# Kernel tuning notes

Hardware: AMD Instinct MI355X
Metric: run time of the kernel (lower is better)

## Reference

```python
import jax, jax.numpy as jnp
import numpy as np
import math

B, S, D, H, HD, BS = 8, 1024, 1024, 16, 64, 8  # batch, seq, dim, heads, head_dim, blk_size
ROPE_BASE = 10000.0


def setup_inputs() -> dict:
    key = jax.random.key(0)
    ks = jax.random.split(key, 5)
    std = 1.0 / math.sqrt(D)
    x = jax.random.normal(ks[0], (B, S, D), dtype=jnp.float32)
    wq = jax.random.normal(ks[1], (D, D), dtype=jnp.float32) * std
    wk = jax.random.normal(ks[2], (D, D), dtype=jnp.float32) * std
    wv = jax.random.normal(ks[3], (D, D), dtype=jnp.float32) * std
    wo = jax.random.normal(ks[4], (D, D), dtype=jnp.float32) * std
    inv_freq = 1.0 / (ROPE_BASE ** (np.arange(0, HD, 2, dtype=np.float32) / HD))
    ang = np.outer(np.arange(S, dtype=np.float32), inv_freq)  # (S, HD/2)
    freqs_cos = jnp.asarray(np.cos(ang), dtype=jnp.float32)
    freqs_sin = jnp.asarray(np.sin(ang), dtype=jnp.float32)
    return {"x": x, "wq": wq, "wk": wk, "wv": wv, "wo": wo,
            "freqs_cos": freqs_cos, "freqs_sin": freqs_sin}


def _rope(t, cos, sin):
    # t: (B, S, H, HD); cos/sin: (S, HD/2); complex-pair rotary (interleaved)
    tr, ti = t[..., 0::2], t[..., 1::2]
    c = cos[None, :, None, :]
    s = sin[None, :, None, :]
    out_r = tr * c - ti * s
    out_i = tr * s + ti * c
    return jnp.stack([out_r, out_i], axis=-1).reshape(t.shape)


def reference(x, wq, wk, wv, wo, freqs_cos, freqs_sin):
    b, s, _ = x.shape
    q = (x @ wq).reshape(b, s, H, HD)
    k = (x @ wk).reshape(b, s, H, HD)
    v = (x @ wv).reshape(b, s, H, HD)
    q = _rope(q, freqs_cos, freqs_sin)
    k = _rope(k, freqs_cos, freqs_sin)
    # block-causal mask: query attends to any key whose block index <= its own
    pos = jnp.arange(s)
    allowed = (pos[None, :] // BS) <= (pos[:, None] // BS)  # (S, S)
    scale = 1.0 / math.sqrt(HD)
    scores = jnp.einsum("bqhd,bkhd->bhqk", q, k) * scale
    scores = jnp.where(allowed[None, None], scores, jnp.finfo(scores.dtype).min)
    probs = jax.nn.softmax(scores, axis=-1)
    out = jnp.einsum("bhqk,bkhd->bqhd", probs, v).reshape(b, s, H * HD)
    return out @ wo
```

## Files before the change

kernel.cpp:

```cpp
#include <hip/hip_runtime.h>
#include <stdint.h>

#define BATCH 8
#define SEQ 1024
#define DMODEL 1024
#define NHEAD 16
#define HDIM 64
#define MROWS (BATCH * SEQ)
#define NQKV (3 * DMODEL)
#define SCALE_LOG2E 0.18033688011112043f

typedef __bf16 bf16x8 __attribute__((ext_vector_type(8)));
typedef float f32x4 __attribute__((ext_vector_type(4)));
typedef unsigned short u16x8 __attribute__((ext_vector_type(8)));
typedef unsigned short u16x4 __attribute__((ext_vector_type(4)));

static __device__ __forceinline__ unsigned short f2bf(float f) {
  unsigned int u = __builtin_bit_cast(unsigned int, f);
  u += 0x7fffu + ((u >> 16) & 1u);
  return (unsigned short)(u >> 16);
}
static __device__ __forceinline__ float bf2f(unsigned short h) {
  unsigned int u = ((unsigned int)h) << 16;
  return __builtin_bit_cast(float, u);
}
static __device__ __forceinline__ void async_cp16(void* lds, const void* g) {
  __builtin_amdgcn_global_load_lds((const __attribute__((address_space(1))) void*)g,
                                   (__attribute__((address_space(3))) void*)lds, 16, 0, 0);
}

__global__ void k_cvt_x(const float* __restrict__ x, unsigned short* __restrict__ xb) {
  const size_t i = ((size_t)blockIdx.x * 256 + threadIdx.x) * 4;
  const float4 v = *(const float4*)(x + i);
  u16x4 o;
  o[0] = f2bf(v.x); o[1] = f2bf(v.y); o[2] = f2bf(v.z); o[3] = f2bf(v.w);
  *(u16x4*)(xb + i) = o;
}

__global__ void k_tpose_tab(const float* __restrict__ fc, const float* __restrict__ fs,
                            float* __restrict__ fcT, float* __restrict__ fsT) {
  const int i = blockIdx.x * 256 + threadIdx.x;
  const int pr = i >> 10, s = i & 1023;
  fcT[i] = fc[s * 32 + pr];
  fsT[i] = fs[s * 32 + pr];
}

__global__ void k_cvt_w(const float* __restrict__ wq, const float* __restrict__ wk,
                        const float* __restrict__ wv, const float* __restrict__ wo,
                        unsigned short* __restrict__ wqkvT, unsigned short* __restrict__ woT) {
  __shared__ float tile[64][65];
  const int z = blockIdx.z;
  const float* w = (z == 0) ? wq : (z == 1) ? wk : (z == 2) ? wv : wo;
  unsigned short* dst = (z < 3) ? (wqkvT + (size_t)z * DMODEL * DMODEL) : woT;
  const int n0 = blockIdx.x * 64, k0 = blockIdx.y * 64;
  for (int i = threadIdx.x; i < 4096; i += 256) {
    const int r = i >> 6, c = i & 63;
    tile[r][c] = w[(size_t)(k0 + r) * DMODEL + n0 + c];
  }
  __syncthreads();
  for (int i = threadIdx.x; i < 4096; i += 256) {
    const int r = i >> 6, c = i & 63;
    dst[(size_t)(n0 + r) * DMODEL + k0 + c] = f2bf(tile[c][r]);
  }
}

template <int NOUT, bool F32OUT>
__global__ __launch_bounds__(256) void k_gemm(const unsigned short* __restrict__ A,
                                              const unsigned short* __restrict__ Bt,
                                              void* __restrict__ Cout) {
  constexpr int K = DMODEL;
  constexpr int GX = NOUT / 128;
  __shared__ unsigned short Al[128 * 32];
  __shared__ unsigned short Bl[128 * 32];
  const int nwg = gridDim.x;
  const int o = blockIdx.x;
  const int t = (o & 7) * (nwg >> 3) + (o >> 3);
  const int tm = (t / GX) * 128, tn = (t % GX) * 128;
  const int tid = threadIdx.x;
  const int lane = tid & 63, wid = tid >> 6;
  const int wm = wid >> 1, wn = wid & 1;
  const int fr = lane & 15, fq = lane >> 4;

  f32x4 acc[4][4];
#pragma unroll
  for (int i = 0; i < 4; ++i)
#pragma unroll
    for (int j = 0; j < 4; ++j) acc[i][j] = (f32x4){0.f, 0.f, 0.f, 0.f};

  const int o0 = wid * 2048 + lane * 16;
  const int row0 = o0 >> 6;
  const int ce0 = (o0 & 63) >> 1;

  for (int kk = 0; kk < K; kk += 32) {
    async_cp16((char*)Al + wid * 2048,        A + (size_t)(tm + row0) * K + kk + ce0);
    async_cp16((char*)Al + wid * 2048 + 1024, A + (size_t)(tm + row0 + 16) * K + kk + ce0);
    async_cp16((char*)Bl + wid * 2048,        Bt + (size_t)(tn + row0) * K + kk + ce0);
    async_cp16((char*)Bl + wid * 2048 + 1024, Bt + (size_t)(tn + row0 + 16) * K + kk + ce0);
    __syncthreads();
    bf16x8 af[4], bf[4];
#pragma unroll
    for (int mi = 0; mi < 4; ++mi)
      af[mi] = *(const bf16x8*)(Al + (wm * 64 + mi * 16 + fr) * 32 + fq * 8);
#pragma unroll
    for (int ni = 0; ni < 4; ++ni)
      bf[ni] = *(const bf16x8*)(Bl + (wn * 64 + ni * 16 + fr) * 32 + fq * 8);
#pragma unroll
    for (int mi = 0; mi < 4; ++mi)
#pragma unroll
      for (int ni = 0; ni < 4; ++ni)
        acc[mi][ni] = __builtin_amdgcn_mfma_f32_16x16x32_bf16(af[mi], bf[ni], acc[mi][ni], 0, 0, 0);
    __syncthreads();
  }

#pragma unroll
  for (int mi = 0; mi < 4; ++mi) {
    const int row = tm + wm * 64 + mi * 16 + fq * 4;
#pragma unroll
    for (int ni = 0; ni < 4; ++ni) {
      const int col = tn + wn * 64 + ni * 16 + fr;
      if constexpr (F32OUT) {
        float* C = (float*)Cout;
#pragma unroll
        for (int r = 0; r < 4; ++r) C[(size_t)(row + r) * NOUT + col] = acc[mi][ni][r];
      } else {
        unsigned short* C = (unsigned short*)Cout;
#pragma unroll
        for (int r = 0; r < 4; ++r) C[(size_t)(row + r) * NOUT + col] = f2bf(acc[mi][ni][r]);
      }
    }
  }
}

__global__ __launch_bounds__(256, 3) void k_gemm_qkv(const unsigned short* __restrict__ A,
                                                     const unsigned short* __restrict__ Bt,
                                                     const float* __restrict__ fcT,
                                                     const float* __restrict__ fsT,
                                                     unsigned short* __restrict__ qr,
                                                     unsigned short* __restrict__ kr,
                                                     unsigned short* __restrict__ vt) {
  constexpr int K = DMODEL;
  constexpr int GX = NQKV / 128;
  __shared__ unsigned short Al[128 * 32];
  __shared__ unsigned short Bl[128 * 32];
  const int nwg = gridDim.x;
  const int o = blockIdx.x;
  const int t = (o & 7) * (nwg >> 3) + (o >> 3);
  const int tm = (t / GX) * 128, tn = (t % GX) * 128;
  const int tid = threadIdx.x;
  const int lane = tid & 63, wid = tid >> 6;
  const int wm = wid >> 1, wn = wid & 1;
  const int fr = lane & 15, fq = lane >> 4;

  f32x4 acc[4][4];
#pragma unroll
  for (int i = 0; i < 4; ++i)
#pragma unroll
    for (int j = 0; j < 4; ++j) acc[i][j] = (f32x4){0.f, 0.f, 0.f, 0.f};

  const int o0 = wid * 2048 + lane * 16;
  const int row0 = o0 >> 6;
  const int ce0 = (o0 & 63) >> 1;

  for (int kk = 0; kk < K; kk += 32) {
    async_cp16((char*)Al + wid * 2048,        A + (size_t)(tm + row0) * K + kk + ce0);
    async_cp16((char*)Al + wid * 2048 + 1024, A + (size_t)(tm + row0 + 16) * K + kk + ce0);
    async_cp16((char*)Bl + wid * 2048,        Bt + (size_t)(tn + row0) * K + kk + ce0);
    async_cp16((char*)Bl + wid * 2048 + 1024, Bt + (size_t)(tn + row0 + 16) * K + kk + ce0);
    __syncthreads();
    bf16x8 af[4], bf[4];
#pragma unroll
    for (int mi = 0; mi < 4; ++mi)
      af[mi] = *(const bf16x8*)(Al + (wm * 64 + mi * 16 + fr) * 32 + fq * 8);
#pragma unroll
    for (int ni = 0; ni < 4; ++ni)
      bf[ni] = *(const bf16x8*)(Bl + (wn * 64 + ni * 16 + fr) * 32 + fq * 8);
#pragma unroll
    for (int mi = 0; mi < 4; ++mi)
#pragma unroll
      for (int ni = 0; ni < 4; ++ni)
        acc[mi][ni] = __builtin_amdgcn_mfma_f32_16x16x32_bf16(af[mi], bf[ni], acc[mi][ni], 0, 0, 0);
    __syncthreads();
  }

  const int typ = tn >> 10;
  const int hh = ((tn & 1023) >> 6) + wn;
  if (typ == 2) {
#pragma unroll
    for (int mi = 0; mi < 4; ++mi) {
      const int rowb = tm + wm * 64 + mi * 16 + fq * 4;
      const int b = rowb >> 10, s0 = rowb & 1023;
#pragma unroll
      for (int ni = 0; ni < 4; ++ni) {
        const int hd = ni * 16 + fr;
        u16x4 ov;
#pragma unroll
        for (int r = 0; r < 4; ++r) ov[r] = f2bf(acc[mi][ni][r]);
        *(u16x4*)(vt + ((size_t)((b * 16 + hh) * 64 + hd)) * SEQ + s0) = ov;
      }
    }
  } else {
    unsigned short* dst = (typ == 0) ? qr : kr;
    const float sgn = (fr & 1) ? 1.0f : -1.0f;
#pragma unroll
    for (int mi = 0; mi < 4; ++mi) {
      const int rowb = tm + wm * 64 + mi * 16 + fq * 4;
      const int b = rowb >> 10, s0 = rowb & 1023;
#pragma unroll
      for (int ni = 0; ni < 4; ++ni) {
        const int hd = ni * 16 + fr;
        const int pr = ni * 8 + (fr >> 1);
        const f32x4 cc = *(const f32x4*)(fcT + (pr << 10) + s0);
        const f32x4 ss = *(const f32x4*)(fsT + (pr << 10) + s0);
#pragma unroll
        for (int r = 0; r < 4; ++r) {
          const float a = acc[mi][ni][r];
          const float p = __shfl_xor(a, 1);
          dst[((size_t)((b * 16 + hh) * SEQ) + s0 + r) * HDIM + hd] = f2bf(a * cc[r] + sgn * (p * ss[r]));
        }
      }
    }
  }
}

__global__ __launch_bounds__(256) void k_attn(const unsigned short* __restrict__ qr,
                                              const unsigned short* __restrict__ kr,
                                              const unsigned short* __restrict__ vt,
                                              unsigned short* __restrict__ ao) {
  const int o = blockIdx.x, nwg = gridDim.x;
  const int t = (o & 7) * (nwg >> 3) + (o >> 3);
  const int qt = 15 - (t & 15);
  const int bh = t >> 4;
  const int tid = threadIdx.x, lane = tid & 63, w = tid >> 6;
  const int fr = lane & 15, fq = lane >> 4;
  __shared__ unsigned short Ks[2][4096];
  __shared__ unsigned short Vs[2][4096];
  __shared__ unsigned short Ps[4][1024];
  const size_t base = (size_t)bh * SEQ * HDIM;
  const char* kgb = (const char*)(kr + base);
  const char* vgb = (const char*)(vt + base);

  const int qrow = qt * 64 + w * 16 + fr;
  const bf16x8 qf0 = *(const bf16x8*)(qr + base + (size_t)qrow * HDIM + fq * 8);
  const bf16x8 qf1 = *(const bf16x8*)(qr + base + (size_t)qrow * HDIM + 32 + fq * 8);
  const int qblk = (w * 16 + fr) >> 3;
  const int swz = (fr & 7) << 4;

  f32x4 oacc[4];
#pragma unroll
  for (int i = 0; i < 4; ++i) oacc[i] = (f32x4){0.f, 0.f, 0.f, 0.f};
  float m = -3.0e38f, l = 0.f;

  auto stage = [&](int kt, int bb) {
#pragma unroll
    for (int c = 0; c < 2; ++c) {
      const int dstb = c * 4096 + tid * 16;
      const int row = dstb >> 7;
      const int col = (dstb & 127) ^ ((row & 7) << 4);
      char* kl = (char*)Ks[bb] + c * 4096 + (tid >> 6) * 1024;
      char* vl = (char*)Vs[bb] + c * 4096 + (tid >> 6) * 1024;
      async_cp16(kl, kgb + (size_t)kt * 8192 + row * 128 + col);
      async_cp16(vl, vgb + (size_t)row * 2048 + kt * 128 + col);
    }
  };

  stage(0, 0);
  int buf = 0;
  for (int kt = 0; kt <= qt; ++kt) {
    const bool pre = (kt < qt);
    if (pre) {
      stage(kt + 1, buf ^ 1);
      asm volatile("s_waitcnt vmcnt(4)" ::: "memory");
    } else {
      asm volatile("s_waitcnt vmcnt(0)" ::: "memory");
    }
    __builtin_amdgcn_s_barrier();
    __builtin_amdgcn_sched_barrier(0);
    const char* Kb = (const char*)Ks[buf];
    const char* Vb = (const char*)Vs[buf];

    f32x4 sc[4];
#pragma unroll
    for (int kb = 0; kb < 4; ++kb) {
      const int rowb = (16 * kb + fr) * 128;
      const bf16x8 k0 = *(const bf16x8*)(Kb + rowb + ((16 * fq) ^ swz));
      const bf16x8 k1 = *(const bf16x8*)(Kb + rowb + ((64 + 16 * fq) ^ swz));
      sc[kb] = __builtin_amdgcn_mfma_f32_16x16x32_bf16(k0, qf0, (f32x4){0.f, 0.f, 0.f, 0.f}, 0, 0, 0);
      sc[kb] = __builtin_amdgcn_mfma_f32_16x16x32_bf16(k1, qf1, sc[kb], 0, 0, 0);
    }
    if (kt == qt) {
#pragma unroll
      for (int kb = 0; kb < 4; ++kb)
        if (2 * kb + (fq >> 1) > qblk) sc[kb] = (f32x4){-3.0e38f, -3.0e38f, -3.0e38f, -3.0e38f};
    }
    float pmax = sc[0][0];
#pragma unroll
    for (int kb = 0; kb < 4; ++kb)
#pragma unroll
      for (int r = 0; r < 4; ++r) pmax = fmaxf(pmax, sc[kb][r]);
    pmax = fmaxf(pmax, __shfl_xor(pmax, 16));
    pmax = fmaxf(pmax, __shfl_xor(pmax, 32));
    const float mnew = fmaxf(m, pmax);
    const float corr = __builtin_amdgcn_exp2f((m - mnew) * SCALE_LOG2E);
    m = mnew;
    float rs = 0.f;
#pragma unroll
    for (int kb = 0; kb < 4; ++kb)
#pragma unroll
      for (int r = 0; r < 4; ++r) {
        const float p = __builtin_amdgcn_exp2f((sc[kb][r] - mnew) * SCALE_LOG2E);
        sc[kb][r] = p;
        rs += p;
      }
    rs += __shfl_xor(rs, 16);
    rs += __shfl_xor(rs, 32);
    l = l * corr + rs;
#pragma unroll
    for (int db = 0; db < 4; ++db) oacc[db] *= corr;
#pragma unroll
    for (int kb = 0; kb < 4; ++kb) {
      u16x4 pv;
#pragma unroll
      for (int r = 0; r < 4; ++r) pv[r] = f2bf(sc[kb][r]);
      *(u16x4*)((char*)Ps[w] + fr * 128 + ((32 * kb + 8 * fq) ^ swz)) = pv;
    }
    asm volatile("s_waitcnt lgkmcnt(0)" ::: "memory");
    __builtin_amdgcn_sched_barrier(0);
    const bf16x8 pf0 = *(const bf16x8*)((const char*)Ps[w] + fr * 128 + ((16 * fq) ^ swz));
    const bf16x8 pf1 = *(const bf16x8*)((const char*)Ps[w] + fr * 128 + ((64 + 16 * fq) ^ swz));
#pragma unroll
    for (int db = 0; db < 4; ++db) {
      const int rowb = (16 * db + fr) * 128;
      const bf16x8 v0 = *(const bf16x8*)(Vb + rowb + ((16 * fq) ^ swz));
      const bf16x8 v1 = *(const bf16x8*)(Vb + rowb + ((64 + 16 * fq) ^ swz));
      oacc[db] = __builtin_amdgcn_mfma_f32_16x16x32_bf16(v0, pf0, oacc[db], 0, 0, 0);
      oacc[db] = __builtin_amdgcn_mfma_f32_16x16x32_bf16(v1, pf1, oacc[db], 0, 0, 0);
    }
    asm volatile("s_waitcnt lgkmcnt(0)" ::: "memory");
    __builtin_amdgcn_sched_barrier(0);
    __builtin_amdgcn_s_barrier();
    buf ^= 1;
  }
  const float inv = 1.f / l;
  const int b = bh >> 4, h = bh & 15;
  const int qg = qt * 64 + w * 16 + fr;
#pragma unroll
  for (int db = 0; db < 4; ++db) {
    u16x4 ov;
#pragma unroll
    for (int r = 0; r < 4; ++r) ov[r] = f2bf(oacc[db][r] * inv);
    *(u16x4*)(ao + (size_t)(b * SEQ + qg) * DMODEL + h * HDIM + 16 * db + 4 * fq) = ov;
  }
}

extern "C" void kernel_launch(void* const* d_in, const int* in_sizes, int n_in,
                              void* d_out, int out_size, void* d_ws, size_t ws_size,
                              hipStream_t stream) {
  (void)in_sizes; (void)n_in; (void)out_size; (void)ws_size;
  const float* x = (const float*)d_in[0];
  const float* wq = (const float*)d_in[1];
  const float* wk = (const float*)d_in[2];
  const float* wv = (const float*)d_in[3];
  const float* wo = (const float*)d_in[4];
  const float* fc = (const float*)d_in[5];
  const float* fs = (const float*)d_in[6];
  float* out = (float*)d_out;

  unsigned short* xb = (unsigned short*)d_ws;
  unsigned short* wqkvT = xb + (size_t)MROWS * DMODEL;
  unsigned short* woT = wqkvT + (size_t)NQKV * DMODEL;
  unsigned short* qrb = woT + (size_t)DMODEL * DMODEL;
  unsigned short* krb = qrb + (size_t)MROWS * DMODEL;
  unsigned short* vtb = krb + (size_t)MROWS * DMODEL;
  float* fcT = (float*)(vtb + (size_t)MROWS * DMODEL);
  float* fsT = fcT + 32 * SEQ;
  unsigned short* aob = xb;

  k_cvt_x<<<MROWS * DMODEL / 1024, 256, 0, stream>>>(x, xb);
  k_tpose_tab<<<128, 256, 0, stream>>>(fc, fs, fcT, fsT);
  k_cvt_w<<<dim3(16, 16, 4), 256, 0, stream>>>(wq, wk, wv, wo, wqkvT, woT);
  k_gemm_qkv<<<(NQKV / 128) * (MROWS / 128), 256, 0, stream>>>(xb, wqkvT, fcT, fsT, qrb, krb, vtb);
  k_attn<<<16 * BATCH * NHEAD, 256, 0, stream>>>(qrb, krb, vtb, aob);
  k_gemm<DMODEL, true><<<(DMODEL / 128) * (MROWS / 128), 256, 0, stream>>>(aob, woT, out);
}
```

Baseline: 257.7 us.

## Merge prep kernels into one launch and widen attention tiles to 128 queries

The three preprocessing kernels (x conversion, weight transpose/convert, rope table transpose) are merged into a single launch dispatched by block index, removing two kernel launches. The attention kernel now uses 512 threads (8 waves) per workgroup covering 128 query rows, so each staged K/V tile is shared by twice as many waves and fewer workgroups are launched. Waves whose rows are entirely masked for a key tile skip compute but still join the barriers, which adds some idle waves on the diagonal tiles and halves the grid size, lowering the count of parallel workgroups.

```diff
diff --git a/kernel.cpp b/kernel.cpp
--- a/kernel.cpp
+++ b/kernel.cpp
@@ -20,47 +20,48 @@
   u += 0x7fffu + ((u >> 16) & 1u);
   return (unsigned short)(u >> 16);
 }
-static __device__ __forceinline__ float bf2f(unsigned short h) {
-  unsigned int u = ((unsigned int)h) << 16;
-  return __builtin_bit_cast(float, u);
-}
 static __device__ __forceinline__ void async_cp16(void* lds, const void* g) {
   __builtin_amdgcn_global_load_lds((const __attribute__((address_space(1))) void*)g,
                                    (__attribute__((address_space(3))) void*)lds, 16, 0, 0);
 }
 
-__global__ void k_cvt_x(const float* __restrict__ x, unsigned short* __restrict__ xb) {
-  const size_t i = ((size_t)blockIdx.x * 256 + threadIdx.x) * 4;
-  const float4 v = *(const float4*)(x + i);
-  u16x4 o;
-  o[0] = f2bf(v.x); o[1] = f2bf(v.y); o[2] = f2bf(v.z); o[3] = f2bf(v.w);
-  *(u16x4*)(xb + i) = o;
-}
-
-__global__ void k_tpose_tab(const float* __restrict__ fc, const float* __restrict__ fs,
-                            float* __restrict__ fcT, float* __restrict__ fsT) {
-  const int i = blockIdx.x * 256 + threadIdx.x;
-  const int pr = i >> 10, s = i & 1023;
-  fcT[i] = fc[s * 32 + pr];
-  fsT[i] = fs[s * 32 + pr];
-}
-
-__global__ void k_cvt_w(const float* __restrict__ wq, const float* __restrict__ wk,
-                        const float* __restrict__ wv, const float* __restrict__ wo,
-                        unsigned short* __restrict__ wqkvT, unsigned short* __restrict__ woT) {
+__global__ __launch_bounds__(256) void k_prep(const float* __restrict__ x,
+                                              const float* __restrict__ wq, const float* __restrict__ wk,
+                                              const float* __restrict__ wv, const float* __restrict__ wo,
+                                              const float* __restrict__ fc, const float* __restrict__ fs,
+                                              unsigned short* __restrict__ xb,
+                                              unsigned short* __restrict__ wqkvT,
+                                              unsigned short* __restrict__ woT,
+                                              float* __restrict__ fcT, float* __restrict__ fsT) {
   __shared__ float tile[64][65];
-  const int z = blockIdx.z;
-  const float* w = (z == 0) ? wq : (z == 1) ? wk : (z == 2) ? wv : wo;
-  unsigned short* dst = (z < 3) ? (wqkvT + (size_t)z * DMODEL * DMODEL) : woT;
-  const int n0 = blockIdx.x * 64, k0 = blockIdx.y * 64;
-  for (int i = threadIdx.x; i < 4096; i += 256) {
-    const int r = i >> 6, c = i & 63;
-    tile[r][c] = w[(size_t)(k0 + r) * DMODEL + n0 + c];
-  }
-  __syncthreads();
-  for (int i = threadIdx.x; i < 4096; i += 256) {
-    const int r = i >> 6, c = i & 63;
-    dst[(size_t)(n0 + r) * DMODEL + k0 + c] = f2bf(tile[c][r]);
+  const int bx = blockIdx.x;
+  const int tid = threadIdx.x;
+  if (bx < 8192) {
+    const size_t i = ((size_t)bx * 256 + tid) * 4;
+    const float4 v = *(const float4*)(x + i);
+    u16x4 o;
+    o[0] = f2bf(v.x); o[1] = f2bf(v.y); o[2] = f2bf(v.z); o[3] = f2bf(v.w);
+    *(u16x4*)(xb + i) = o;
+  } else if (bx < 9216) {
+    const int idx = bx - 8192;
+    const int z = idx >> 8;
+    const float* w = (z == 0) ? wq : (z == 1) ? wk : (z == 2) ? wv : wo;
+    unsigned short* dst = (z < 3) ? (wqkvT + (size_t)z * DMODEL * DMODEL) : woT;
+    const int n0 = (idx & 15) * 64, k0 = ((idx >> 4) & 15) * 64;
+    for (int i = tid; i < 4096; i += 256) {
+      const int r = i >> 6, c = i & 63;
+      tile[r][c] = w[(size_t)(k0 + r) * DMODEL + n0 + c];
+    }
+    __syncthreads();
+    for (int i = tid; i < 4096; i += 256) {
+      const int r = i >> 6, c = i & 63;
+      dst[(size_t)(n0 + r) * DMODEL + k0 + c] = f2bf(tile[c][r]);
+    }
+  } else {
+    const int i = (bx - 9216) * 256 + tid;
+    const int pr = i >> 10, s = i & 1023;
+    fcT[i] = fc[s * 32 + pr];
+    fsT[i] = fs[s * 32 + pr];
   }
 }
 
@@ -222,27 +223,28 @@
   }
 }
 
-__global__ __launch_bounds__(256) void k_attn(const unsigned short* __restrict__ qr,
+__global__ __launch_bounds__(512) void k_attn(const unsigned short* __restrict__ qr,
                                               const unsigned short* __restrict__ kr,
                                               const unsigned short* __restrict__ vt,
                                               unsigned short* __restrict__ ao) {
   const int o = blockIdx.x, nwg = gridDim.x;
   const int t = (o & 7) * (nwg >> 3) + (o >> 3);
-  const int qt = 15 - (t & 15);
-  const int bh = t >> 4;
+  const int qt2 = 7 - (t & 7);
+  const int bh = t >> 3;
   const int tid = threadIdx.x, lane = tid & 63, w = tid >> 6;
   const int fr = lane & 15, fq = lane >> 4;
   __shared__ unsigned short Ks[2][4096];
   __shared__ unsigned short Vs[2][4096];
-  __shared__ unsigned short Ps[4][1024];
+  __shared__ unsigned short Ps[8][1024];
   const size_t base = (size_t)bh * SEQ * HDIM;
   const char* kgb = (const char*)(kr + base);
   const char* vgb = (const char*)(vt + base);
 
-  const int qrow = qt * 64 + w * 16 + fr;
+  const int qmin = qt2 * 128 + w * 16;
+  const int qrow = qmin + fr;
   const bf16x8 qf0 = *(const bf16x8*)(qr + base + (size_t)qrow * HDIM + fq * 8);
   const bf16x8 qf1 = *(const bf16x8*)(qr + base + (size_t)qrow * HDIM + 32 + fq * 8);
-  const int qblk = (w * 16 + fr) >> 3;
+  const int qblk8 = qrow >> 3;
   const int swz = (fr & 7) << 4;
 
   f32x4 oacc[4];
@@ -251,25 +253,22 @@
   float m = -3.0e38f, l = 0.f;
 
   auto stage = [&](int kt, int bb) {
-#pragma unroll
-    for (int c = 0; c < 2; ++c) {
-      const int dstb = c * 4096 + tid * 16;
-      const int row = dstb >> 7;
-      const int col = (dstb & 127) ^ ((row & 7) << 4);
-      char* kl = (char*)Ks[bb] + c * 4096 + (tid >> 6) * 1024;
-      char* vl = (char*)Vs[bb] + c * 4096 + (tid >> 6) * 1024;
-      async_cp16(kl, kgb + (size_t)kt * 8192 + row * 128 + col);
-      async_cp16(vl, vgb + (size_t)row * 2048 + kt * 128 + col);
-    }
+    const int dstb = tid * 16;
+    const int row = dstb >> 7;
+    const int col = (dstb & 127) ^ ((row & 7) << 4);
+    char* kl = (char*)Ks[bb] + (tid >> 6) * 1024;
+    char* vl = (char*)Vs[bb] + (tid >> 6) * 1024;
+    async_cp16(kl, kgb + (size_t)kt * 8192 + row * 128 + col);
+    async_cp16(vl, vgb + (size_t)row * 2048 + kt * 128 + col);
   };
 
+  const int ktmax = 2 * qt2 + 1;
   stage(0, 0);
   int buf = 0;
-  for (int kt = 0; kt <= qt; ++kt) {
-    const bool pre = (kt < qt);
-    if (pre) {
+  for (int kt = 0; kt <= ktmax; ++kt) {
+    if (kt < ktmax) {
       stage(kt + 1, buf ^ 1);
-      asm volatile("s_waitcnt vmcnt(4)" ::: "memory");
+      asm volatile("s_waitcnt vmcnt(2)" ::: "memory");
     } else {
       asm volatile("s_waitcnt vmcnt(0)" ::: "memory");
     }
@@ -278,77 +277,79 @@
     const char* Kb = (const char*)Ks[buf];
     const char* Vb = (const char*)Vs[buf];
 
-    f32x4 sc[4];
-#pragma unroll
-    for (int kb = 0; kb < 4; ++kb) {
-      const int rowb = (16 * kb + fr) * 128;
-      const bf16x8 k0 = *(const bf16x8*)(Kb + rowb + ((16 * fq) ^ swz));
-      const bf16x8 k1 = *(const bf16x8*)(Kb + rowb + ((64 + 16 * fq) ^ swz));
-      sc[kb] = __builtin_amdgcn_mfma_f32_16x16x32_bf16(k0, qf0, (f32x4){0.f, 0.f, 0.f, 0.f}, 0, 0, 0);
-      sc[kb] = __builtin_amdgcn_mfma_f32_16x16x32_bf16(k1, qf1, sc[kb], 0, 0, 0);
-    }
-    if (kt == qt) {
+    if (kt * 64 <= qmin + 15) {
+      f32x4 sc[4];
+#pragma unroll
+      for (int kb = 0; kb < 4; ++kb) {
+        const int rowb = (16 * kb + fr) * 128;
+        const bf16x8 k0 = *(const bf16x8*)(Kb + rowb + ((16 * fq) ^ swz));
+        const bf16x8 k1 = *(const bf16x8*)(Kb + rowb + ((64 + 16 * fq) ^ swz));
+        sc[kb] = __builtin_amdgcn_mfma_f32_16x16x32_bf16(k0, qf0, (f32x4){0.f, 0.f, 0.f, 0.f}, 0, 0, 0);
+        sc[kb] = __builtin_amdgcn_mfma_f32_16x16x32_bf16(k1, qf1, sc[kb], 0, 0, 0);
+      }
+      if (kt * 64 + 56 > qmin) {
+#pragma unroll
+        for (int kb = 0; kb < 4; ++kb)
+          if (8 * kt + 2 * kb + (fq >> 1) > qblk8)
+            sc[kb] = (f32x4){-3.0e38f, -3.0e38f, -3.0e38f, -3.0e38f};
+      }
+      float pmax = sc[0][0];
 #pragma unroll
       for (int kb = 0; kb < 4; ++kb)
-        if (2 * kb + (fq >> 1) > qblk) sc[kb] = (f32x4){-3.0e38f, -3.0e38f, -3.0e38f, -3.0e38f};
-    }
-    float pmax = sc[0][0];
-#pragma unroll
-    for (int kb = 0; kb < 4; ++kb)
-#pragma unroll
-      for (int r = 0; r < 4; ++r) pmax = fmaxf(pmax, sc[kb][r]);
-    pmax = fmaxf(pmax, __shfl_xor(pmax, 16));
-    pmax = fmaxf(pmax, __shfl_xor(pmax, 32));
-    const float mnew = fmaxf(m, pmax);
-    const float corr = __builtin_amdgcn_exp2f((m - mnew) * SCALE_LOG2E);
-    m = mnew;
-    float rs = 0.f;
-#pragma unroll
-    for (int kb = 0; kb < 4; ++kb)
-#pragma unroll
-      for (int r = 0; r < 4; ++r) {
-        const float p = __builtin_amdgcn_exp2f((sc[kb][r] - mnew) * SCALE_LOG2E);
-        sc[kb][r] = p;
-        rs += p;
-      }
-    rs += __shfl_xor(rs, 16);
-    rs += __shfl_xor(rs, 32);
-    l = l * corr + rs;
-#pragma unroll
-    for (int db = 0; db < 4; ++db) oacc[db] *= corr;
-#pragma unroll
-    for (int kb = 0; kb < 4; ++kb) {
-      u16x4 pv;
-#pragma unroll
-      for (int r = 0; r < 4; ++r) pv[r] = f2bf(sc[kb][r]);
-      *(u16x4*)((char*)Ps[w] + fr * 128 + ((32 * kb + 8 * fq) ^ swz)) = pv;
-    }
-    asm volatile("s_waitcnt lgkmcnt(0)" ::: "memory");
-    __builtin_amdgcn_sched_barrier(0);
-    const bf16x8 pf0 = *(const bf16x8*)((const char*)Ps[w] + fr * 128 + ((16 * fq) ^ swz));
-    const bf16x8 pf1 = *(const bf16x8*)((const char*)Ps[w] + fr * 128 + ((64 + 16 * fq) ^ swz));
-#pragma unroll
-    for (int db = 0; db < 4; ++db) {
-      const int rowb = (16 * db + fr) * 128;
-      const bf16x8 v0 = *(const bf16x8*)(Vb + rowb + ((16 * fq) ^ swz));
-      const bf16x8 v1 = *(const bf16x8*)(Vb + rowb + ((64 + 16 * fq) ^ swz));
-      oacc[db] = __builtin_amdgcn_mfma_f32_16x16x32_bf16(v0, pf0, oacc[db], 0, 0, 0);
-      oacc[db] = __builtin_amdgcn_mfma_f32_16x16x32_bf16(v1, pf1, oacc[db], 0, 0, 0);
-    }
-    asm volatile("s_waitcnt lgkmcnt(0)" ::: "memory");
-    __builtin_amdgcn_sched_barrier(0);
+#pragma unroll
+        for (int r = 0; r < 4; ++r) pmax = fmaxf(pmax, sc[kb][r]);
+      pmax = fmaxf(pmax, __shfl_xor(pmax, 16));
+      pmax = fmaxf(pmax, __shfl_xor(pmax, 32));
+      const float mnew = fmaxf(m, pmax);
+      const float corr = __builtin_amdgcn_exp2f((m - mnew) * SCALE_LOG2E);
+      m = mnew;
+      float rs = 0.f;
+#pragma unroll
+      for (int kb = 0; kb < 4; ++kb)
+#pragma unroll
+        for (int r = 0; r < 4; ++r) {
+          const float p = __builtin_amdgcn_exp2f((sc[kb][r] - mnew) * SCALE_LOG2E);
+          sc[kb][r] = p;
+          rs += p;
+        }
+      rs += __shfl_xor(rs, 16);
+      rs += __shfl_xor(rs, 32);
+      l = l * corr + rs;
+#pragma unroll
+      for (int db = 0; db < 4; ++db) oacc[db] *= corr;
+#pragma unroll
+      for (int kb = 0; kb < 4; ++kb) {
+        u16x4 pv;
+#pragma unroll
+        for (int r = 0; r < 4; ++r) pv[r] = f2bf(sc[kb][r]);
+        *(u16x4*)((char*)Ps[w] + fr * 128 + ((32 * kb + 8 * fq) ^ swz)) = pv;
+      }
+      asm volatile("s_waitcnt lgkmcnt(0)" ::: "memory");
+      __builtin_amdgcn_sched_barrier(0);
+      const bf16x8 pf0 = *(const bf16x8*)((const char*)Ps[w] + fr * 128 + ((16 * fq) ^ swz));
+      const bf16x8 pf1 = *(const bf16x8*)((const char*)Ps[w] + fr * 128 + ((64 + 16 * fq) ^ swz));
+#pragma unroll
+      for (int db = 0; db < 4; ++db) {
+        const int rowb = (16 * db + fr) * 128;
+        const bf16x8 v0 = *(const bf16x8*)(Vb + rowb + ((16 * fq) ^ swz));
+        const bf16x8 v1 = *(const bf16x8*)(Vb + rowb + ((64 + 16 * fq) ^ swz));
+        oacc[db] = __builtin_amdgcn_mfma_f32_16x16x32_bf16(v0, pf0, oacc[db], 0, 0, 0);
+        oacc[db] = __builtin_amdgcn_mfma_f32_16x16x32_bf16(v1, pf1, oacc[db], 0, 0, 0);
+      }
+      asm volatile("s_waitcnt lgkmcnt(0)" ::: "memory");
+      __builtin_amdgcn_sched_barrier(0);
+    }
     __builtin_amdgcn_s_barrier();
     buf ^= 1;
   }
   const float inv = 1.f / l;
   const int b = bh >> 4, h = bh & 15;
-  const int qg = qt * 64 + w * 16 + fr;
 #pragma unroll
   for (int db = 0; db < 4; ++db) {
     u16x4 ov;
 #pragma unroll
     for (int r = 0; r < 4; ++r) ov[r] = f2bf(oacc[db][r] * inv);
-    *(u16x4*)(ao + (size_t)(b * SEQ + qg) * DMODEL + h * HDIM + 16 * db + 4 * fq) = ov;
+    *(u16x4*)(ao + (size_t)(b * SEQ + qrow) * DMODEL + h * HDIM + 16 * db + 4 * fq) = ov;
   }
 }
 
@@ -375,10 +376,8 @@
   float* fsT = fcT + 32 * SEQ;
   unsigned short* aob = xb;
 
-  k_cvt_x<<<MROWS * DMODEL / 1024, 256, 0, stream>>>(x, xb);
-  k_tpose_tab<<<128, 256, 0, stream>>>(fc, fs, fcT, fsT);
-  k_cvt_w<<<dim3(16, 16, 4), 256, 0, stream>>>(wq, wk, wv, wo, wqkvT, woT);
+  k_prep<<<9344, 256, 0, stream>>>(x, wq, wk, wv, wo, fc, fs, xb, wqkvT, woT, fcT, fsT);
   k_gemm_qkv<<<(NQKV / 128) * (MROWS / 128), 256, 0, stream>>>(xb, wqkvT, fcT, fsT, qrb, krb, vtb);
-  k_attn<<<16 * BATCH * NHEAD, 256, 0, stream>>>(qrb, krb, vtb, aob);
+  k_attn<<<8 * BATCH * NHEAD, 512, 0, stream>>>(qrb, krb, vtb, aob);
   k_gemm<DMODEL, true><<<(DMODEL / 128) * (MROWS / 128), 256, 0, stream>>>(aob, woT, out);
 }
```

Result: faster. 248.9 us (-3.4%).
